# Optimization experiments

Hardware: AMD Instinct MI355X
Metric: run time of the kernel (lower is better)

## Reference

```python
import jax, jax.numpy as jnp
import numpy as np

BATCH, K, N = 16384, 512, 1024  # codewords, message_length, code_length


def setup_inputs() -> dict:
    key = jax.random.key(0)
    kx, km = jax.random.split(key)
    # binary message bits as float32 (as the torch module casts with .float())
    x = jnp.round(jax.random.uniform(kx, (BATCH, K), dtype=jnp.float32))
    # binary polar generator matrix [K, N]
    matrix = jnp.round(jax.random.uniform(km, (K, N), dtype=jnp.float32))
    return {"x": x, "matrix": matrix}


def reference(x, matrix):
    # GF(2) encoding: (x @ G) mod 2, returned as integer codeword bits
    codeword = jnp.remainder(x @ matrix, 2.0)
    return codeword.astype(jnp.int32)
```

## Files before the change

kernel.cpp:

```cpp
#include <hip/hip_runtime.h>
#include <stdint.h>

#define BATCH 16384
#define KDIM  512
#define NDIM  1024
#define NW    16
#define THREADS 512
#define ROWS_PER_BLOCK 16
#define PHASE_ROWS 4
#define NPHASE (ROWS_PER_BLOCK / PHASE_ROWS)

__global__ __launch_bounds__(256) void pack_g_kernel(const float* __restrict__ G,
                                                     uint32_t* __restrict__ Gt) {
    int t = blockIdx.x * 256 + threadIdx.x;
    int n = t & (NDIM - 1);
    int m = t >> 10;
    int kbase = 256 * (m >> 3) + 128 * ((m >> 2) & 1) + (m & 3);
    uint32_t w = 0;
#pragma unroll
    for (int c = 0; c < 32; ++c) {
        w |= (uint32_t)(G[(size_t)(kbase + 4 * c) * NDIM + n] > 0.5f) << c;
    }
    Gt[t] = w;
}

__global__ __launch_bounds__(THREADS, 6)
void gf2_fused_kernel(const float* __restrict__ x,
                      const uint32_t* __restrict__ Gt,
                      int* __restrict__ out) {
    const int tid = threadIdx.x;
    const int w   = tid >> 6;
    const int l   = tid & 63;
    const int q   = w >> 1;
    const int h   = w & 1;
    const int row0 = blockIdx.x * ROWS_PER_BLOCK;

    uint32_t g0[NW], g1[NW];
#pragma unroll
    for (int m = 0; m < NW; ++m) {
        uint2 gg = reinterpret_cast<const uint2*>(Gt + m * NDIM)[tid];
        g0[m] = gg.x;
        g1[m] = gg.y;
    }

    __shared__ __align__(16) uint32_t xw[2][PHASE_ROWS][NW];

    const float4* xf = reinterpret_cast<const float4*>(x);
    float4 f = xf[(size_t)row0 * (KDIM / 4) + tid];

    for (int p = 0; p < NPHASE; ++p) {
        uint64_t b0 = __ballot(f.x > 0.5f);
        uint64_t b1 = __ballot(f.y > 0.5f);
        uint64_t b2 = __ballot(f.z > 0.5f);
        uint64_t b3 = __ballot(f.w > 0.5f);

        if (p + 1 < NPHASE)
            f = xf[(size_t)(row0 + (p + 1) * PHASE_ROWS) * (KDIM / 4) + tid];

        if (l == 0) {
            uint32_t* dst = &xw[p & 1][q][h * 8];
            dst[0] = (uint32_t)b0;  dst[4] = (uint32_t)(b0 >> 32);
            dst[1] = (uint32_t)b1;  dst[5] = (uint32_t)(b1 >> 32);
            dst[2] = (uint32_t)b2;  dst[6] = (uint32_t)(b2 >> 32);
            dst[3] = (uint32_t)b3;  dst[7] = (uint32_t)(b3 >> 32);
        }
        __syncthreads();

        size_t obase = (size_t)(row0 + p * PHASE_ROWS) * NDIM + 2 * (size_t)tid;
#pragma unroll
        for (int r = 0; r < PHASE_ROWS; ++r) {
            const uint4* x4 = reinterpret_cast<const uint4*>(&xw[p & 1][r][0]);
            uint4 a0 = x4[0], a1 = x4[1], a2 = x4[2], a3 = x4[3];
            uint32_t t0 = (a0.x & g0[0])  ^ (a0.y & g0[1])  ^ (a0.z & g0[2])  ^ (a0.w & g0[3])
                        ^ (a1.x & g0[4])  ^ (a1.y & g0[5])  ^ (a1.z & g0[6])  ^ (a1.w & g0[7])
                        ^ (a2.x & g0[8])  ^ (a2.y & g0[9])  ^ (a2.z & g0[10]) ^ (a2.w & g0[11])
                        ^ (a3.x & g0[12]) ^ (a3.y & g0[13]) ^ (a3.z & g0[14]) ^ (a3.w & g0[15]);
            uint32_t t1 = (a0.x & g1[0])  ^ (a0.y & g1[1])  ^ (a0.z & g1[2])  ^ (a0.w & g1[3])
                        ^ (a1.x & g1[4])  ^ (a1.y & g1[5])  ^ (a1.z & g1[6])  ^ (a1.w & g1[7])
                        ^ (a2.x & g1[8])  ^ (a2.y & g1[9])  ^ (a2.z & g1[10]) ^ (a2.w & g1[11])
                        ^ (a3.x & g1[12]) ^ (a3.y & g1[13]) ^ (a3.z & g1[14]) ^ (a3.w & g1[15]);
            int2 o;
            o.x = (int)(__popc(t0) & 1u);
            o.y = (int)(__popc(t1) & 1u);
            *reinterpret_cast<int2*>(out + obase + (size_t)r * NDIM) = o;
        }
    }
}

extern "C" void kernel_launch(void* const* d_in, const int* in_sizes, int n_in,
                              void* d_out, int out_size, void* d_ws, size_t ws_size,
                              hipStream_t stream) {
    const float* x = (const float*)d_in[0];
    const float* G = (const float*)d_in[1];
    int* out = (int*)d_out;

    uint32_t* Gt = (uint32_t*)d_ws;

    pack_g_kernel<<<(NW * NDIM) / 256, 256, 0, stream>>>(G, Gt);
    gf2_fused_kernel<<<BATCH / ROWS_PER_BLOCK, THREADS, 0, stream>>>(x, Gt, out);
}
```

Baseline: 27.43 us.

## Parallelize G packing across more threads and use nontemporal loads/stores

The packing kernel now splits each 32-bit word across 8 threads of 4 bits each and merges the partial words through shared memory. This gives 512 blocks instead of 64 and shortens the serial chain of dependent loads per thread. The main kernel switches its streaming x loads and output stores to nontemporal builtins, so the one-touch traffic does not pollute cache. Costs are an added syncthreads with a shared-memory reduction in the pack kernel, and cache-policy effects that may be neutral on this hardware.

Result: slower. 34.04 us (+24.1%).

```diff
diff --git a/kernel.cpp b/kernel.cpp
--- a/kernel.cpp
+++ b/kernel.cpp
@@ -10,18 +10,33 @@
 #define PHASE_ROWS 4
 #define NPHASE (ROWS_PER_BLOCK / PHASE_ROWS)
 
+typedef float f32x4 __attribute__((ext_vector_type(4)));
+typedef int   i32x2 __attribute__((ext_vector_type(2)));
+
 __global__ __launch_bounds__(256) void pack_g_kernel(const float* __restrict__ G,
                                                      uint32_t* __restrict__ Gt) {
-    int t = blockIdx.x * 256 + threadIdx.x;
-    int n = t & (NDIM - 1);
-    int m = t >> 10;
-    int kbase = 256 * (m >> 3) + 128 * ((m >> 2) & 1) + (m & 3);
+    __shared__ uint32_t nib[8][32];
+    const int bid = blockIdx.x;
+    const int m   = bid >> 5;
+    const int n0  = (bid & 31) << 5;
+    const int tid = threadIdx.x;
+    const int p   = tid >> 5;
+    const int nn  = tid & 31;
+    const int n   = n0 + nn;
+    const int kbase = 256 * (m >> 3) + 128 * ((m >> 2) & 1) + (m & 3);
     uint32_t w = 0;
 #pragma unroll
-    for (int c = 0; c < 32; ++c) {
+    for (int j = 0; j < 4; ++j) {
+        int c = 4 * p + j;
         w |= (uint32_t)(G[(size_t)(kbase + 4 * c) * NDIM + n] > 0.5f) << c;
     }
-    Gt[t] = w;
+    nib[p][nn] = w;
+    __syncthreads();
+    if (tid < 32) {
+        uint32_t r = nib[0][tid] | nib[1][tid] | nib[2][tid] | nib[3][tid]
+                   | nib[4][tid] | nib[5][tid] | nib[6][tid] | nib[7][tid];
+        Gt[m * NDIM + n0 + tid] = r;
+    }
 }
 
 __global__ __launch_bounds__(THREADS, 6)
@@ -45,8 +60,8 @@
 
     __shared__ __align__(16) uint32_t xw[2][PHASE_ROWS][NW];
 
-    const float4* xf = reinterpret_cast<const float4*>(x);
-    float4 f = xf[(size_t)row0 * (KDIM / 4) + tid];
+    const f32x4* xf = reinterpret_cast<const f32x4*>(x);
+    f32x4 f = __builtin_nontemporal_load(xf + (size_t)row0 * (KDIM / 4) + tid);
 
     for (int p = 0; p < NPHASE; ++p) {
         uint64_t b0 = __ballot(f.x > 0.5f);
@@ -55,7 +70,8 @@
         uint64_t b3 = __ballot(f.w > 0.5f);
 
         if (p + 1 < NPHASE)
-            f = xf[(size_t)(row0 + (p + 1) * PHASE_ROWS) * (KDIM / 4) + tid];
+            f = __builtin_nontemporal_load(
+                    xf + (size_t)(row0 + (p + 1) * PHASE_ROWS) * (KDIM / 4) + tid);
 
         if (l == 0) {
             uint32_t* dst = &xw[p & 1][q][h * 8];
@@ -79,10 +95,11 @@
                         ^ (a1.x & g1[4])  ^ (a1.y & g1[5])  ^ (a1.z & g1[6])  ^ (a1.w & g1[7])
                         ^ (a2.x & g1[8])  ^ (a2.y & g1[9])  ^ (a2.z & g1[10]) ^ (a2.w & g1[11])
                         ^ (a3.x & g1[12]) ^ (a3.y & g1[13]) ^ (a3.z & g1[14]) ^ (a3.w & g1[15]);
-            int2 o;
+            i32x2 o;
             o.x = (int)(__popc(t0) & 1u);
             o.y = (int)(__popc(t1) & 1u);
-            *reinterpret_cast<int2*>(out + obase + (size_t)r * NDIM) = o;
+            __builtin_nontemporal_store(
+                o, reinterpret_cast<i32x2*>(out + obase + (size_t)r * NDIM));
         }
     }
 }
@@ -96,6 +113,6 @@
 
     uint32_t* Gt = (uint32_t*)d_ws;
 
-    pack_g_kernel<<<(NW * NDIM) / 256, 256, 0, stream>>>(G, Gt);
+    pack_g_kernel<<<512, 256, 0, stream>>>(G, Gt);
     gf2_fused_kernel<<<BATCH / ROWS_PER_BLOCK, THREADS, 0, stream>>>(x, Gt, out);
 }
```
